# Optimization experiments

Measured on AMD Instinct MI355X. Metric: run time of the kernel, lower is better.

## Reference

```python
import jax, jax.numpy as jnp
import numpy as np

B, T, C, H, N = 2, 1024, 2048, 32, 64
LAYER_ID, N_LAYERS = 12, 24
EPS = 1e-5 * 8 ** 2  # GroupNorm eps = 1e-5 * head_size_divisor**2


def setup_inputs() -> dict:
    key = jax.random.key(0)
    ks = jax.random.split(key, 16)
    nrm = lambda i, shape, s: jax.random.normal(ks[i], shape, jnp.float32) * s
    r01 = LAYER_ID / (N_LAYERS - 1)
    r1a0 = 1.0 - LAYER_ID / N_LAYERS
    ddd = (jnp.arange(C, dtype=jnp.float32) / C)[None, None, :]
    nn_ = jnp.arange(C, dtype=jnp.float32) / (C - 1)
    decay_speed = -7.0 + 5.0 * nn_ ** (0.85 + r01 ** 0.5)
    lin_s = 1.0 / float(np.sqrt(C))
    inp = dict(
        x=nrm(0, (B, T, C), 1.0),
        v_first=nrm(1, (B, T, C), 1.0),
        shift_state=jnp.zeros((B, C), jnp.float32),
        wkv_state=jnp.zeros((B, H, N, N), jnp.float32),
        x_r=1.0 - ddd ** (0.2 * r1a0),
        x_w=1.0 - ddd ** (0.9 * r1a0),
        x_k=1.0 - (ddd ** (0.9 * r1a0) + 0.4 * r01),
        x_v=1.0 - (ddd ** (0.4 * r1a0) + 0.6 * r01),
        x_a=1.0 - ddd ** (0.9 * r1a0),
        x_g=1.0 - ddd ** (0.2 * r1a0),
        w0=decay_speed[None, None, :] + 0.5,
        w1=nrm(2, (C, 64), 0.05), w2=nrm(3, (64, C), 0.1),
        a0=jnp.zeros((1, 1, C), jnp.float32),
        a1=nrm(4, (C, 64), 0.05), a2=nrm(5, (64, C), 0.1),
        v0=jnp.ones((1, 1, C), jnp.float32),
        v1=nrm(6, (C, 32), 0.05), v2=nrm(7, (32, C), 0.1),
        g1=nrm(8, (C, 128), 0.05), g2=nrm(9, (128, C), 0.1),
        k_k=jnp.full((1, 1, C), 0.85, jnp.float32),
        k_a=jnp.ones((1, 1, C), jnp.float32),
        r_k=nrm(10, (H, N), 0.02),
        W_r=nrm(11, (C, C), lin_s), W_k=nrm(12, (C, C), lin_s),
        W_v=nrm(13, (C, C), lin_s), W_o=nrm(14, (C, C), lin_s),
        ln_w=jnp.ones((C,), jnp.float32), ln_b=jnp.zeros((C,), jnp.float32),
    )
    return inp


def _forward(x, v_first, shift_state, wkv_state, x_r, x_w, x_k, x_v, x_a, x_g,
             w0, w1, w2, a0, a1, a2, v0, v1, v2, g1, g2, k_k, k_a, r_k,
             W_r, W_k, W_v, W_o, ln_w, ln_b):
    # token shift
    xx = jnp.concatenate([shift_state[:, None, :], x[:, :-1]], axis=1) - x
    xr, xw, xk, xv, xa, xg = (x + xx * m for m in (x_r, x_w, x_k, x_v, x_a, x_g))
    r = xr @ W_r
    k = xk @ W_k
    v = xv @ W_v
    # log-decay (strictly negative)
    w_log = -jax.nn.softplus(-(w0 + jnp.tanh(xw @ w1) @ w2)) - 0.5
    # residual value mixing towards layer-0 v (layer_id > 0 branch)
    v = v + (v_first - v) * jax.nn.sigmoid(v0 + xv @ v1 @ v2)
    a = jax.nn.sigmoid(a0 + xa @ a1 @ a2)
    g = jax.nn.sigmoid(xg @ g1) @ g2
    # per-head L2-normalized removal key
    kk = (k * k_k).reshape(B, T, H, N)
    kk = kk / jnp.maximum(jnp.linalg.norm(kk, axis=-1, keepdims=True), 1e-12)
    k2 = k * (1.0 + (a - 1.0) * k_a)
    # time-major [T,B,H,N] for the scan
    tm = lambda t: t.reshape(B, T, H, N).transpose(1, 0, 2, 3)
    rs, ks_, vs = tm(r), tm(k2), tm(v)
    ws = jnp.exp(tm(w_log))               # per-channel decay in (0,1)
    a_in = -kk.transpose(1, 0, 2, 3)      # removal direction
    b_in = (kk * a.reshape(B, T, H, N)).transpose(1, 0, 2, 3)
    def step(S, t):  # S: [B,H,Nv,Nk]
        r_, k_, v_, w_, a_, b_ = t
        sa = jnp.einsum('bhvk,bhk->bhv', S, a_)
        S = S * w_[:, :, None, :] \
            + jnp.einsum('bhv,bhk->bhvk', sa, b_) \
            + jnp.einsum('bhv,bhk->bhvk', v_, k_)
        return S, jnp.einsum('bhvk,bhk->bhv', S, r_)
    S_final, o = jax.lax.scan(step, wkv_state, (rs, ks_, vs, ws, a_in, b_in))
    o = o.transpose(1, 0, 2, 3)           # [B,T,H,N]
    # GroupNorm with H groups over C channels (per-head normalization)
    mu = o.mean(-1, keepdims=True)
    var = ((o - mu) ** 2).mean(-1, keepdims=True)
    on = ((o - mu) / jnp.sqrt(var + EPS)).reshape(B, T, C) * ln_w + ln_b
    # rkv bonus term
    rr, kr, vr = r.reshape(B, T, H, N), k2.reshape(B, T, H, N), v.reshape(B, T, H, N)
    bonus = ((rr * kr * r_k).sum(-1, keepdims=True) * vr).reshape(B, T, C)
    out = ((on + bonus) * g) @ W_o
    return out


def reference(x, v_first, shift_state, wkv_state, x_r, x_w, x_k, x_v, x_a, x_g,
              w0, w1, w2, a0, a1, a2, v0, v1, v2, g1, g2, k_k, k_a, r_k,
              W_r, W_k, W_v, W_o, ln_w, ln_b):
    return _forward(x, v_first, shift_state, wkv_state, x_r, x_w, x_k, x_v, x_a, x_g,
                    w0, w1, w2, a0, a1, a2, v0, v1, v2, g1, g2, k_k, k_a, r_k,
                    W_r, W_k, W_v, W_o, ln_w, ln_b)
```

## Files before the change

### kernel.cpp

```cpp
#include <hip/hip_runtime.h>
#include <cstdint>
#include <cstddef>


#define DI __device__ __forceinline__
static constexpr int T_ = 1024, C_ = 2048, H_ = 32;

typedef __attribute__((ext_vector_type(8))) __bf16 bf16x8;
typedef __attribute__((ext_vector_type(4))) float f32x4;
typedef __attribute__((ext_vector_type(8))) unsigned short us8v;
typedef __attribute__((ext_vector_type(4))) unsigned short us4v;
typedef __attribute__((ext_vector_type(2))) unsigned short us2v;

DI float sig_(float z) { return 1.0f / (1.0f + expf(-z)); }

DI unsigned short f2bf(float f) {
  union { float f; uint32_t u; } v; v.f = f;
  uint32_t u = v.u;
  return (unsigned short)((u + 0x7FFFu + ((u >> 16) & 1u)) >> 16);
}
DI float bf2f(unsigned short h) {
  union { uint32_t u; float f; } v; v.u = ((uint32_t)h) << 16;
  return v.f;
}

DI float dpp_xor1_add(float x) {
  int r = __builtin_amdgcn_update_dpp(0, __float_as_int(x), 0xB1, 0xF, 0xF, true);
  return x + __int_as_float(r);
}
DI float dpp_xor2_add(float x) {
  int r = __builtin_amdgcn_update_dpp(0, __float_as_int(x), 0x4E, 0xF, 0xF, true);
  return x + __int_as_float(r);
}
DI float dpp_hm_add(float x) {
  int r = __builtin_amdgcn_update_dpp(0, __float_as_int(x), 0x141, 0xF, 0xF, true);
  return x + __int_as_float(r);
}

DI void gload16(const float* g, float* l) {
  __builtin_amdgcn_global_load_lds(
      (const __attribute__((address_space(1))) uint32_t*)g,
      (__attribute__((address_space(3))) uint32_t*)l, 16, 0, 0);
}
DI void gload16u(const unsigned short* g, unsigned short* l) {
  __builtin_amdgcn_global_load_lds(
      (const __attribute__((address_space(1))) uint32_t*)g,
      (__attribute__((address_space(3))) uint32_t*)l, 16, 0, 0);
}
DI void gload4(const float* g, float* l) {
  __builtin_amdgcn_global_load_lds(
      (const __attribute__((address_space(1))) uint32_t*)g,
      (__attribute__((address_space(3))) uint32_t*)l, 4, 0, 0);
}

struct Job {
  const float* A; const float* W; float* C; const float* bias;
  const float* mixv; const float* x; const float* shift;
  int N, K, ntn, aact, epi, tile_end;
};
struct Jobs { Job j[7]; };

__global__ __launch_bounds__(256) void gemm_oracle(Jobs P) {
  __shared__ float As[64][33];
  __shared__ float Ws[32][65];
  int bx = blockIdx.x, ji = 0;
  while (bx >= P.j[ji].tile_end) ++ji;
  Job J = P.j[ji];
  int tix = bx - (ji ? P.j[ji - 1].tile_end : 0);
  int mt = tix / J.ntn, nt = tix % J.ntn;
  int m0 = mt * 64, n0 = nt * 64;
  int tid = threadIdx.x, tx = tid & 15, ty = tid >> 4;
  float acc[4][4] = {};
  for (int k0 = 0; k0 < J.K; k0 += 32) {
    #pragma unroll
    for (int p = 0; p < 8; ++p) {
      int idx = p * 256 + tid;
      int r = idx >> 5, kc = idx & 31;
      int m = m0 + r, k = k0 + kc;
      float a;
      if (J.mixv) {
        float xv = J.x[(size_t)m * C_ + k];
        int t = m & (T_ - 1);
        float xp = (t == 0) ? J.shift[(size_t)(m >> 10) * C_ + k]
                            : J.x[(size_t)(m - 1) * C_ + k];
        a = xv + (xp - xv) * J.mixv[k];
      } else {
        a = J.A[(size_t)m * J.K + k];
        if (J.aact == 1) a = tanhf(a);
        else if (J.aact == 2) a = sig_(a);
      }
      As[r][kc] = a;
    }
    #pragma unroll
    for (int p = 0; p < 8; ++p) {
      int idx = p * 256 + tid;
      int kr = idx >> 6, nc = idx & 63;
      int n = n0 + nc;
      Ws[kr][nc] = (n < J.N) ? J.W[(size_t)(k0 + kr) * J.N + n] : 0.0f;
    }
    __syncthreads();
    #pragma unroll 4
    for (int kc = 0; kc < 32; ++kc) {
      float av[4], bv[4];
      #pragma unroll
      for (int i = 0; i < 4; ++i) av[i] = As[ty * 4 + i][kc];
      #pragma unroll
      for (int jn = 0; jn < 4; ++jn) bv[jn] = Ws[kc][tx * 4 + jn];
      #pragma unroll
      for (int i = 0; i < 4; ++i)
        #pragma unroll
        for (int jn = 0; jn < 4; ++jn) acc[i][jn] += av[i] * bv[jn];
    }
    __syncthreads();
  }
  #pragma unroll
  for (int i = 0; i < 4; ++i) {
    int rw = m0 + ty * 4 + i;
    #pragma unroll
    for (int jn = 0; jn < 4; ++jn) {
      int col = n0 + tx * 4 + jn;
      if (col < J.N) {
        float v = acc[i][jn];
        if (J.epi == 1) v = sig_(J.bias[col] + v);
        else if (J.epi == 2) v = 0.60653065971263342f * sig_(J.bias[col] + v);
        if (J.epi == 3) ((unsigned short*)J.C)[(size_t)rw * J.N + col] = f2bf(v);
        else            J.C[(size_t)rw * J.N + col] = v;
      }
    }
  }
}

struct TJob { const float* src; unsigned short* dh; unsigned short* dl; int N, ntn, tile_end; };
struct TJobs { TJob j[8]; };

__global__ __launch_bounds__(256) void wtrans(TJobs P) {
  __shared__ float t[64][65];
  int bx = blockIdx.x, ji = 0;
  while (bx >= P.j[ji].tile_end) ++ji;
  TJob J = P.j[ji];
  int tix = bx - (ji ? P.j[ji - 1].tile_end : 0);
  int kt = tix / J.ntn, nt = tix % J.ntn;
  int k0 = kt * 64, n0 = nt * 64;
  int tid = threadIdx.x;
  #pragma unroll
  for (int p = 0; p < 16; ++p) {
    int flat = p * 256 + tid;
    int r = flat >> 6, c = flat & 63;
    int n = n0 + c;
    t[r][c] = (n < J.N) ? J.src[(size_t)(k0 + r) * J.N + n] : 0.0f;
  }
  __syncthreads();
  #pragma unroll
  for (int p = 0; p < 8; ++p) {
    int flat = p * 256 + tid;
    int rr = flat >> 5, cc = (flat & 31) * 2;
    if (n0 + rr < J.N) {
      float w0v = t[cc][rr], w1v = t[cc + 1][rr];
      unsigned short h0 = f2bf(w0v), h1 = f2bf(w1v);
      us2v oh, ol;
      oh.x = h0; oh.y = h1;
      ol.x = f2bf(w0v - bf2f(h0));
      ol.y = f2bf(w1v - bf2f(h1));
      size_t off = (size_t)(n0 + rr) * 2048 + k0 + cc;
      *(us2v*)(J.dh + off) = oh;
      *(us2v*)(J.dl + off) = ol;
    }
  }
}

struct GJob {
  const float* A; const unsigned short* Wh; const unsigned short* Wl; float* C;
  const float* mixv; const float* shift;
  int N, K, ntn, kbeg, kend, atomicC, tile_end;
};
struct GJobs { GJob j[8]; };

__global__ __launch_bounds__(256, 2) void gemm_w256(GJobs P) {
  __shared__ unsigned short Ash[128][40];
  __shared__ unsigned short Asl[128][40];
  __shared__ unsigned short Bsh[256][32];
  __shared__ unsigned short Bsl[256][32];
  int bx = blockIdx.x, ji = 0;
  while (bx >= P.j[ji].tile_end) ++ji;
  GJob J = P.j[ji];
  int tix = bx - (ji ? P.j[ji - 1].tile_end : 0);
  int mt = tix / J.ntn, nt = tix % J.ntn;
  int m0 = mt * 128, n0 = nt * 256;
  int tid = threadIdx.x;
  int lane = tid & 63, wid = tid >> 6;
  int wr = wid >> 1, wc = wid & 1;
  int l15 = lane & 15, lg = lane >> 4;
  f32x4 acc[4][8] = {};

  int sr = tid >> 3, skq = tid & 7;
  float ax[4][4], aq[4][4], amv[4];

  auto loadA = [&](int k0) {
    int kk = k0 + skq * 4;
    if (J.mixv) *(float4*)amv = *(const float4*)(J.mixv + kk);
    #pragma unroll
    for (int p = 0; p < 4; ++p) {
      int m = m0 + p * 32 + sr;
      const float* xp0 = J.A + (size_t)m * J.K + kk;
      *(float4*)ax[p] = *(const float4*)xp0;
      if (J.mixv) {
        const float* pp = ((m & (T_ - 1)) == 0)
            ? (J.shift + (size_t)(m >> 10) * C_ + kk)
            : (xp0 - C_);
        *(float4*)aq[p] = *(const float4*)pp;
      }
    }
  };
  auto writeA = [&]() {
    #pragma unroll
    for (int p = 0; p < 4; ++p) {
      us4v oh, ol;
      #pragma unroll
      for (int q = 0; q < 4; ++q) {
        float va = J.mixv ? (ax[p][q] + (aq[p][q] - ax[p][q]) * amv[q]) : ax[p][q];
        unsigned short hq = f2bf(va);
        oh[q] = hq;
        ol[q] = f2bf(va - bf2f(hq));
      }
      int r = p * 32 + sr;
      *(us4v*)&Ash[r][skq * 4] = oh;
      *(us4v*)&Asl[r][skq * 4] = ol;
    }
  };
  auto stageB = [&](int k0) {
    #pragma unroll
    for (int j = 0; j < 4; ++j) {
      int r0 = wid * 64 + j * 16;
      int nrow = n0 + r0 + (lane >> 2);
      if (nrow >= J.N) nrow = J.N - 1;
      size_t gofs = (size_t)nrow * J.K + k0 + (lane & 3) * 8;
      gload16u(J.Wh + gofs, &Bsh[r0][0]);
      gload16u(J.Wl + gofs, &Bsl[r0][0]);
    }
  };

  loadA(J.kbeg);
  stageB(J.kbeg);
  writeA();
  asm volatile("s_waitcnt vmcnt(0)" ::: "memory");
  __syncthreads();

  for (int k0 = J.kbeg; k0 < J.kend; k0 += 32) {
    bool more = (k0 + 32 < J.kend);
    if (more) loadA(k0 + 32);
    bf16x8 afh[4], afl[4];
    #pragma unroll
    for (int i = 0; i < 4; ++i) {
      int rr = wr * 64 + i * 16 + l15;
      afh[i] = __builtin_bit_cast(bf16x8, *(const us8v*)&Ash[rr][lg * 8]);
      afl[i] = __builtin_bit_cast(bf16x8, *(const us8v*)&Asl[rr][lg * 8]);
    }
    #pragma unroll
    for (int jn = 0; jn < 8; ++jn) {
      int rb = wc * 128 + jn * 16 + l15;
      bf16x8 bh = __builtin_bit_cast(bf16x8, *(const us8v*)&Bsh[rb][lg * 8]);
      bf16x8 bl = __builtin_bit_cast(bf16x8, *(const us8v*)&Bsl[rb][lg * 8]);
      #pragma unroll
      for (int i = 0; i < 4; ++i) {
        acc[i][jn] = __builtin_amdgcn_mfma_f32_16x16x32_bf16(afh[i], bh, acc[i][jn], 0, 0, 0);
        acc[i][jn] = __builtin_amdgcn_mfma_f32_16x16x32_bf16(afl[i], bh, acc[i][jn], 0, 0, 0);
        acc[i][jn] = __builtin_amdgcn_mfma_f32_16x16x32_bf16(afh[i], bl, acc[i][jn], 0, 0, 0);
      }
    }
    __syncthreads();
    if (more) { stageB(k0 + 32); writeA(); }
    asm volatile("s_waitcnt vmcnt(0)" ::: "memory");
    __syncthreads();
  }

  int orow0 = m0 + wr * 64 + 4 * lg;
  int ocol0 = n0 + wc * 128 + l15;
  #pragma unroll
  for (int i = 0; i < 4; ++i) {
    #pragma unroll
    for (int jn = 0; jn < 8; ++jn) {
      int col = ocol0 + jn * 16;
      if (col < J.N) {
        #pragma unroll
        for (int rr = 0; rr < 4; ++rr) {
          size_t idx = (size_t)(orow0 + i * 16 + rr) * J.N + col;
          float v = acc[i][jn][rr];
          if (J.atomicC) atomicAdd(&J.C[idx], v);
          else           J.C[idx] = v;
        }
      }
    }
  }
}

__global__ __launch_bounds__(64) void prescan(
    float* __restrict__ kio, float* __restrict__ vio,
    float* __restrict__ amat_ain, float* __restrict__ vmix_bin,
    const float* __restrict__ vfirst,
    const float* __restrict__ k_k, const float* __restrict__ k_a) {
  __shared__ float red[64];
  int bid = blockIdx.x, tid = threadIdx.x;
  int h = bid & (H_ - 1);
  size_t base = (size_t)bid * 64 + tid;
  int cc = h * 64 + tid;
  float kv = kio[base];
  float kkv = kv * k_k[cc];
  red[tid] = kkv * kkv;
  __syncthreads();
  for (int s = 32; s > 0; s >>= 1) { if (tid < s) red[tid] += red[tid + s]; __syncthreads(); }
  float nrm = fmaxf(sqrtf(red[0]), 1e-12f);
  float kkn = kkv / nrm;
  float av = amat_ain[base];
  float vmv = vmix_bin[base];
  float vv = vio[base];
  kio[base] = kv * (1.0f + (av - 1.0f) * k_a[cc]);
  vio[base] = vv + (vfirst[base] - vv) * vmv;
  amat_ain[base] = -kkn;
  vmix_bin[base] = kkn * av;
}

static constexpr int CH = 16;

#define LOADSTEP(BUF, S_, Aa, Ww, Kk, Bb, Rr, Vt)                  \
  {                                                                \
    *(float4*)&Aa[0] = *(const float4*)&lds[BUF][3][S_][kb];       \
    *(float4*)&Aa[4] = *(const float4*)&lds[BUF][3][S_][kb + 4];   \
    *(float4*)&Ww[0] = *(const float4*)&lds[BUF][2][S_][kb];       \
    *(float4*)&Ww[4] = *(const float4*)&lds[BUF][2][S_][kb + 4];   \
    *(float4*)&Kk[0] = *(const float4*)&lds[BUF][1][S_][kb];       \
    *(float4*)&Kk[4] = *(const float4*)&lds[BUF][1][S_][kb + 4];   \
    *(float4*)&Bb[0] = *(const float4*)&lds[BUF][4][S_][kb];       \
    *(float4*)&Bb[4] = *(const float4*)&lds[BUF][4][S_][kb + 4];   \
    *(float4*)&Rr[0] = *(const float4*)&lds[BUF][0][S_][kb];       \
    *(float4*)&Rr[4] = *(const float4*)&lds[BUF][0][S_][kb + 4];   \
    Vt = vtl[BUF][S_][vl];                                         \
  }

#define COMPSTEP(Aa, Ww, Kk, Bb, Rr, Vt, TIDX)                              \
  {                                                                         \
    float p0 = S[0] * Aa[0], p1 = S[1] * Aa[1];                             \
    float p2 = S[2] * Aa[2], p3 = S[3] * Aa[3];                             \
    p0 = fmaf(S[4], Aa[4], p0); p1 = fmaf(S[5], Aa[5], p1);                 \
    p2 = fmaf(S[6], Aa[6], p2); p3 = fmaf(S[7], Aa[7], p3);                 \
    float sa = (p0 + p1) + (p2 + p3);                                       \
    sa = dpp_xor1_add(sa);                                                  \
    sa = dpp_xor2_add(sa);                                                  \
    sa = dpp_hm_add(sa);                                                    \
    float y0 = 0.f, y1 = 0.f, y2 = 0.f, y3 = 0.f;                           \
    _Pragma("unroll") for (int i = 0; i < 8; i += 4) {                      \
      S[i]     = fmaf(S[i],     Ww[i],     fmaf(Vt, Kk[i],     sa * Bb[i])); \
      S[i + 1] = fmaf(S[i + 1], Ww[i + 1], fmaf(Vt, Kk[i + 1], sa * Bb[i + 1])); \
      S[i + 2] = fmaf(S[i + 2], Ww[i + 2], fmaf(Vt, Kk[i + 2], sa * Bb[i + 2])); \
      S[i + 3] = fmaf(S[i + 3], Ww[i + 3], fmaf(Vt, Kk[i + 3], sa * Bb[i + 3])); \
      y0 = fmaf(S[i], Rr[i], y0);                                           \
      y1 = fmaf(S[i + 1], Rr[i + 1], y1);                                   \
      y2 = fmaf(S[i + 2], Rr[i + 2], y2);                                   \
      y3 = fmaf(S[i + 3], Rr[i + 3], y3);                                   \
    }                                                                       \
    float y = (y0 + y1) + (y2 + y3);                                        \
    y = dpp_xor1_add(y);                                                    \
    y = dpp_xor2_add(y);                                                    \
    y = dpp_hm_add(y);                                                      \
    if (kq == 0) obf[bh + (size_t)(TIDX)*2048 + v0 + vl] = f2bf(y);         \
  }

__global__ __launch_bounds__(64) void wkv_scan_v5(
    const float* __restrict__ r, const float* __restrict__ k2,
    const float* __restrict__ w, const float* __restrict__ ain,
    const float* __restrict__ bin, const float* __restrict__ vp,
    const float* __restrict__ sInit, unsigned short* __restrict__ obf) {
  __shared__ float lds[2][5][CH][64];
  __shared__ float vtl[2][CH][8];
  int D = blockIdx.x;
  int chain = (D & 7) + 8 * (D >> 6);
  int vblk = (D >> 3) & 7;
  int b = chain >> 5, h = chain & 31;
  int v0 = vblk * 8;
  int lane = threadIdx.x;
  int vl = lane >> 3, kq = lane & 7;
  int kb = kq * 8;
  size_t bh = (size_t)(b * T_) * 2048 + (size_t)h * 64;

  float S[8];
  {
    const float* sp = sInit + (((size_t)chain * 64 + v0 + vl) * 64) + kb;
    float4 s0 = *(const float4*)(sp);
    float4 s1 = *(const float4*)(sp + 4);
    S[0] = s0.x; S[1] = s0.y; S[2] = s0.z; S[3] = s0.w;
    S[4] = s1.x; S[5] = s1.y; S[6] = s1.z; S[7] = s1.w;
  }

  const float* arr[5] = {r, k2, w, ain, bin};

  auto stage = [&](int buf, int t0) {
    #pragma unroll
    for (int a = 0; a < 5; ++a) {
      #pragma unroll
      for (int jj = 0; jj < 4; ++jj) {
        size_t gofs = bh + (size_t)(t0 + jj * 4 + (lane >> 4)) * 2048 + (lane & 15) * 4;
        gload16(arr[a] + gofs, &lds[buf][a][jj * 4][0]);
      }
    }
    #pragma unroll
    for (int di = 0; di < 2; ++di) {
      size_t gofs = bh + (size_t)(t0 + di * 8 + (lane >> 3)) * 2048 + v0 + (lane & 7);
      gload4(vp + gofs, &vtl[buf][di * 8][0]);
    }
  };

  stage(0, 0);
  asm volatile("s_waitcnt vmcnt(0)" ::: "memory");

  float A0[8], W0[8], K0[8], B0[8], R0[8], vt0;
  float A1[8], W1[8], K1[8], B1[8], R1[8], vt1;

  for (int c = 0; c < T_ / CH; ++c) {
    int cur = c & 1;
    if (c + 1 < T_ / CH) stage(cur ^ 1, (c + 1) * CH);
    int t0 = c * CH;
    LOADSTEP(cur, 0, A0, W0, K0, B0, R0, vt0);
    #pragma unroll 2
    for (int s = 0; s < CH; s += 2) {
      LOADSTEP(cur, s + 1, A1, W1, K1, B1, R1, vt1);
      COMPSTEP(A0, W0, K0, B0, R0, vt0, t0 + s);
      if (s + 2 < CH) LOADSTEP(cur, s + 2, A0, W0, K0, B0, R0, vt0);
      COMPSTEP(A1, W1, K1, B1, R1, vt1, t0 + s + 1);
    }
    asm volatile("s_waitcnt vmcnt(0)" ::: "memory");
  }
}

__global__ __launch_bounds__(64) void post(
    const unsigned short* __restrict__ obf, const float* __restrict__ r,
    const float* __restrict__ k2, const float* __restrict__ vp,
    const unsigned short* __restrict__ gbf, const float* __restrict__ r_k,
    const float* __restrict__ lnw, const float* __restrict__ lnb,
    float* __restrict__ afin) {
  __shared__ float red[64];
  int bid = blockIdx.x, tid = threadIdx.x;
  int h = bid & 31;
  size_t base = (size_t)bid * 64 + tid;
  int cc = h * 64 + tid;
  float ov = bf2f(obf[base]);
  red[tid] = ov; __syncthreads();
  for (int s = 32; s > 0; s >>= 1) { if (tid < s) red[tid] += red[tid + s]; __syncthreads(); }
  float mu = red[0] * (1.0f / 64.0f);
  __syncthreads();
  float dv = ov - mu;
  red[tid] = dv * dv; __syncthreads();
  for (int s = 32; s > 0; s >>= 1) { if (tid < s) red[tid] += red[tid + s]; __syncthreads(); }
  float var = red[0] * (1.0f / 64.0f);
  __syncthreads();
  float on = dv * rsqrtf(var + 6.4e-4f) * lnw[cc] + lnb[cc];
  float pr = r[base] * k2[base] * r_k[cc];
  red[tid] = pr; __syncthreads();
  for (int s = 32; s > 0; s >>= 1) { if (tid < s) red[tid] += red[tid + s]; __syncthreads(); }
  float dot = red[0];
  float val = (on + dot * vp[base]) * bf2f(gbf[base]);
  afin[base] = val;
}

static constexpr size_t KB = 1024;
static constexpr size_t O_R    = 0;
static constexpr size_t O_K    = 16384;
static constexpr size_t O_V    = 32768;
static constexpr size_t O_WDEC = 49152;
static constexpr size_t O_AMAT = 65536;
static constexpr size_t O_VMIX = 81920;
static constexpr size_t O_AIN  = O_AMAT;
static constexpr size_t O_BIN  = O_VMIX;
static constexpr size_t O_AFIN = O_VMIX;
static constexpr size_t O_WRT_H = 49152, O_WRT_L = 57344;
static constexpr size_t O_WKT_H = 65536, O_WKT_L = 73728;
static constexpr size_t O_WVT_H = 81920, O_WVT_L = 90112;
static constexpr size_t O_W1T_H = 98304, O_W1T_L = 98560;
static constexpr size_t O_A1T_H = 98816, O_A1T_L = 99072;
static constexpr size_t O_V1T_H = 99328, O_V1T_L = 99456;
static constexpr size_t O_G1T_H = 99584, O_G1T_L = 100096;
static constexpr size_t O_WOT_H = 0, O_WOT_L = 8192;

extern "C" void kernel_launch(void* const* d_in, const int* in_sizes, int n_in,
                              void* d_out, int out_size, void* d_ws, size_t ws_size,
                              hipStream_t stream) {
  const float* x      = (const float*)d_in[0];
  const float* vfirst = (const float*)d_in[1];
  const float* shift  = (const float*)d_in[2];
  const float* wkv0   = (const float*)d_in[3];
  const float* x_r = (const float*)d_in[4];
  const float* x_w = (const float*)d_in[5];
  const float* x_k = (const float*)d_in[6];
  const float* x_v = (const float*)d_in[7];
  const float* x_a = (const float*)d_in[8];
  const float* x_g = (const float*)d_in[9];
  const float* w0 = (const float*)d_in[10];
  const float* w1 = (const float*)d_in[11];
  const float* w2 = (const float*)d_in[12];
  const float* a0 = (const float*)d_in[13];
  const float* a1 = (const float*)d_in[14];
  const float* a2 = (const float*)d_in[15];
  const float* v0 = (const float*)d_in[16];
  const float* v1 = (const float*)d_in[17];
  const float* v2 = (const float*)d_in[18];
  const float* g1 = (const float*)d_in[19];
  const float* g2 = (const float*)d_in[20];
  const float* k_k = (const float*)d_in[21];
  const float* k_a = (const float*)d_in[22];
  const float* r_k = (const float*)d_in[23];
  const float* W_r = (const float*)d_in[24];
  const float* W_k = (const float*)d_in[25];
  const float* W_v = (const float*)d_in[26];
  const float* W_o = (const float*)d_in[27];
  const float* ln_w = (const float*)d_in[28];
  const float* ln_b = (const float*)d_in[29];

  char* ws = (char*)d_ws;
  auto F = [&](size_t kb) { return (float*)(ws + kb * KB); };
  auto U = [&](size_t kb) { return (unsigned short*)(ws + kb * KB); };
  float* outp = (float*)d_out;
  unsigned short* gbf = (unsigned short*)d_out;
  unsigned short* obf = (unsigned short*)((char*)d_out + 8192 * KB);
  float* HW2 = (float*)((char*)d_out + 8192 * KB);
  float* HA2 = (float*)((char*)d_out + 8704 * KB);
  float* HV2 = (float*)((char*)d_out + 9216 * KB);
  float* HG2 = (float*)((char*)d_out + 9472 * KB);

  {
    TJobs TG{};
    int cum = 0, i = 0;
    auto addT = [&](const float* src, size_t hkb, size_t lkb, int N) {
      int ntn = (N + 63) / 64;
      cum += 32 * ntn;
      TG.j[i++] = TJob{src, U(hkb), U(lkb), N, ntn, cum};
    };
    addT(W_r, O_WRT_H, O_WRT_L, 2048);
    addT(W_k, O_WKT_H, O_WKT_L, 2048);
    addT(W_v, O_WVT_H, O_WVT_L, 2048);
    addT(w1, O_W1T_H, O_W1T_L, 64);
    addT(a1, O_A1T_H, O_A1T_L, 64);
    addT(v1, O_V1T_H, O_V1T_L, 32);
    addT(g1, O_G1T_H, O_G1T_L, 128);
    wtrans<<<dim3(cum), dim3(256), 0, stream>>>(TG);
  }

  {
    GJobs G{};
    int cum = 0, i = 0;
    auto add = [&](size_t hkb, size_t lkb, float* Cp, const float* mixv, int N) {
      int ntn = (N + 255) / 256;
      cum += 16 * ntn;
      G.j[i++] = GJob{x, U(hkb), U(lkb), Cp, mixv, shift, N, 2048, ntn, 0, 2048, 0, cum};
    };
    add(O_WRT_H, O_WRT_L, F(O_R), x_r, 2048);
    add(O_WKT_H, O_WKT_L, F(O_K), x_k, 2048);
    add(O_WVT_H, O_WVT_L, F(O_V), x_v, 2048);
    add(O_W1T_H, O_W1T_L, HW2, x_w, 64);
    add(O_A1T_H, O_A1T_L, HA2, x_a, 64);
    add(O_V1T_H, O_V1T_L, HV2, x_v, 32);
    add(O_G1T_H, O_G1T_L, HG2, x_g, 128);
    gemm_w256<<<dim3(cum), dim3(256), 0, stream>>>(G);
  }

  {
    Jobs G{};
    int cum = 0, i = 0;
    auto add = [&](const float* A, const float* W, float* C, const float* bias,
                   int K, int aact, int epi) {
      cum += 32 * 32;
      G.j[i++] = Job{A, W, C, bias, nullptr, nullptr, nullptr, 2048, K, 32, aact, epi, cum};
    };
    add(HW2, w2, F(O_WDEC), w0, 64, 1, 2);
    add(HA2, a2, F(O_AMAT), a0, 64, 0, 1);
    add(HV2, v2, F(O_VMIX), v0, 32, 0, 1);
    add(HG2, g2, (float*)gbf, nullptr, 128, 2, 3);
    gemm_oracle<<<dim3(cum), dim3(256), 0, stream>>>(G);
  }

  prescan<<<dim3(65536), dim3(64), 0, stream>>>(F(O_K), F(O_V), F(O_AMAT), F(O_VMIX),
                                                vfirst, k_k, k_a);

  wkv_scan_v5<<<dim3(512), dim3(64), 0, stream>>>(F(O_R), F(O_K), F(O_WDEC), F(O_AIN),
                                                  F(O_BIN), F(O_V), wkv0, obf);

  post<<<dim3(65536), dim3(64), 0, stream>>>(obf, F(O_R), F(O_K), F(O_V),
                                             gbf, r_k, ln_w, ln_b, F(O_AFIN));

  hipMemsetAsync(d_out, 0, (size_t)16384 * KB, stream);

  {
    TJobs TO{};
    TO.j[0] = TJob{W_o, U(O_WOT_H), U(O_WOT_L), 2048, 32, 1024};
    wtrans<<<dim3(1024), dim3(256), 0, stream>>>(TO);
  }

  {
    GJobs G{};
    G.j[0] = GJob{F(O_AFIN), U(O_WOT_H), U(O_WOT_L), outp, nullptr, nullptr,
                  2048, 2048, 8, 0, 1024, 1, 128};
    G.j[1] = GJob{F(O_AFIN), U(O_WOT_H), U(O_WOT_L), outp, nullptr, nullptr,
                  2048, 2048, 8, 1024, 2048, 1, 256};
    gemm_w256<<<dim3(256), dim3(256), 0, stream>>>(G);
  }

  (void)in_sizes; (void)n_in; (void)out_size; (void)ws_size;
}
```

Before: 866.2 us.

## Split WKV scan across more blocks with four state columns per lane

The recurrent WKV scan now gives each wave 4 value rows instead of 8, with 16 lanes each holding 4 key entries, and launches 1024 single-wave blocks instead of 512. The per-step serial chain per lane gets shorter (4 FMAs instead of 8) and more CUs run in parallel on the latency-bound scan. The cost is one extra DPP reduction stage per step, each chunk's inputs being loaded twice as many times overall, and a chunk size halved to 8, which doubles the number of barrier/waitcnt points.

```diff
diff --git a/kernel.cpp b/kernel.cpp
--- a/kernel.cpp
+++ b/kernel.cpp
@@ -34,6 +34,10 @@
 }
 DI float dpp_hm_add(float x) {
   int r = __builtin_amdgcn_update_dpp(0, __float_as_int(x), 0x141, 0xF, 0xF, true);
+  return x + __int_as_float(r);
+}
+DI float dpp_mir_add(float x) {
+  int r = __builtin_amdgcn_update_dpp(0, __float_as_int(x), 0x140, 0xF, 0xF, true);
   return x + __int_as_float(r);
 }
 
@@ -319,75 +323,65 @@
   vmix_bin[base] = kkn * av;
 }
 
-static constexpr int CH = 16;
+static constexpr int CH = 8;
 
 #define LOADSTEP(BUF, S_, Aa, Ww, Kk, Bb, Rr, Vt)                  \
   {                                                                \
     *(float4*)&Aa[0] = *(const float4*)&lds[BUF][3][S_][kb];       \
-    *(float4*)&Aa[4] = *(const float4*)&lds[BUF][3][S_][kb + 4];   \
     *(float4*)&Ww[0] = *(const float4*)&lds[BUF][2][S_][kb];       \
-    *(float4*)&Ww[4] = *(const float4*)&lds[BUF][2][S_][kb + 4];   \
     *(float4*)&Kk[0] = *(const float4*)&lds[BUF][1][S_][kb];       \
-    *(float4*)&Kk[4] = *(const float4*)&lds[BUF][1][S_][kb + 4];   \
     *(float4*)&Bb[0] = *(const float4*)&lds[BUF][4][S_][kb];       \
-    *(float4*)&Bb[4] = *(const float4*)&lds[BUF][4][S_][kb + 4];   \
     *(float4*)&Rr[0] = *(const float4*)&lds[BUF][0][S_][kb];       \
-    *(float4*)&Rr[4] = *(const float4*)&lds[BUF][0][S_][kb + 4];   \
     Vt = vtl[BUF][S_][vl];                                         \
   }
 
 #define COMPSTEP(Aa, Ww, Kk, Bb, Rr, Vt, TIDX)                              \
   {                                                                         \
     float p0 = S[0] * Aa[0], p1 = S[1] * Aa[1];                             \
-    float p2 = S[2] * Aa[2], p3 = S[3] * Aa[3];                             \
-    p0 = fmaf(S[4], Aa[4], p0); p1 = fmaf(S[5], Aa[5], p1);                 \
-    p2 = fmaf(S[6], Aa[6], p2); p3 = fmaf(S[7], Aa[7], p3);                 \
-    float sa = (p0 + p1) + (p2 + p3);                                       \
+    p0 = fmaf(S[2], Aa[2], p0);                                             \
+    p1 = fmaf(S[3], Aa[3], p1);                                             \
+    float sa = p0 + p1;                                                     \
     sa = dpp_xor1_add(sa);                                                  \
     sa = dpp_xor2_add(sa);                                                  \
     sa = dpp_hm_add(sa);                                                    \
-    float y0 = 0.f, y1 = 0.f, y2 = 0.f, y3 = 0.f;                           \
-    _Pragma("unroll") for (int i = 0; i < 8; i += 4) {                      \
-      S[i]     = fmaf(S[i],     Ww[i],     fmaf(Vt, Kk[i],     sa * Bb[i])); \
-      S[i + 1] = fmaf(S[i + 1], Ww[i + 1], fmaf(Vt, Kk[i + 1], sa * Bb[i + 1])); \
-      S[i + 2] = fmaf(S[i + 2], Ww[i + 2], fmaf(Vt, Kk[i + 2], sa * Bb[i + 2])); \
-      S[i + 3] = fmaf(S[i + 3], Ww[i + 3], fmaf(Vt, Kk[i + 3], sa * Bb[i + 3])); \
-      y0 = fmaf(S[i], Rr[i], y0);                                           \
-      y1 = fmaf(S[i + 1], Rr[i + 1], y1);                                   \
-      y2 = fmaf(S[i + 2], Rr[i + 2], y2);                                   \
-      y3 = fmaf(S[i + 3], Rr[i + 3], y3);                                   \
-    }                                                                       \
-    float y = (y0 + y1) + (y2 + y3);                                        \
+    sa = dpp_mir_add(sa);                                                   \
+    S[0] = fmaf(S[0], Ww[0], fmaf(Vt, Kk[0], sa * Bb[0]));                  \
+    S[1] = fmaf(S[1], Ww[1], fmaf(Vt, Kk[1], sa * Bb[1]));                  \
+    S[2] = fmaf(S[2], Ww[2], fmaf(Vt, Kk[2], sa * Bb[2]));                  \
+    S[3] = fmaf(S[3], Ww[3], fmaf(Vt, Kk[3], sa * Bb[3]));                  \
+    float y0 = S[0] * Rr[0], y1 = S[1] * Rr[1];                             \
+    y0 = fmaf(S[2], Rr[2], y0);                                             \
+    y1 = fmaf(S[3], Rr[3], y1);                                             \
+    float y = y0 + y1;                                                      \
     y = dpp_xor1_add(y);                                                    \
     y = dpp_xor2_add(y);                                                    \
     y = dpp_hm_add(y);                                                      \
+    y = dpp_mir_add(y);                                                     \
     if (kq == 0) obf[bh + (size_t)(TIDX)*2048 + v0 + vl] = f2bf(y);         \
   }
 
-__global__ __launch_bounds__(64) void wkv_scan_v5(
+__global__ __launch_bounds__(64) void wkv_scan_v6(
     const float* __restrict__ r, const float* __restrict__ k2,
     const float* __restrict__ w, const float* __restrict__ ain,
     const float* __restrict__ bin, const float* __restrict__ vp,
     const float* __restrict__ sInit, unsigned short* __restrict__ obf) {
   __shared__ float lds[2][5][CH][64];
-  __shared__ float vtl[2][CH][8];
+  __shared__ float vtl[2][16][4];
   int D = blockIdx.x;
-  int chain = (D & 7) + 8 * (D >> 6);
-  int vblk = (D >> 3) & 7;
+  int chain = (D & 7) + 8 * (D >> 7);
+  int vblk = (D >> 3) & 15;
   int b = chain >> 5, h = chain & 31;
-  int v0 = vblk * 8;
+  int v0 = vblk * 4;
   int lane = threadIdx.x;
-  int vl = lane >> 3, kq = lane & 7;
-  int kb = kq * 8;
+  int vl = lane >> 4, kq = lane & 15;
+  int kb = kq * 4;
   size_t bh = (size_t)(b * T_) * 2048 + (size_t)h * 64;
 
-  float S[8];
+  float S[4];
   {
     const float* sp = sInit + (((size_t)chain * 64 + v0 + vl) * 64) + kb;
-    float4 s0 = *(const float4*)(sp);
-    float4 s1 = *(const float4*)(sp + 4);
+    float4 s0 = *(const float4*)sp;
     S[0] = s0.x; S[1] = s0.y; S[2] = s0.z; S[3] = s0.w;
-    S[4] = s1.x; S[5] = s1.y; S[6] = s1.z; S[7] = s1.w;
   }
 
   const float* arr[5] = {r, k2, w, ain, bin};
@@ -396,23 +390,24 @@
     #pragma unroll
     for (int a = 0; a < 5; ++a) {
       #pragma unroll
-      for (int jj = 0; jj < 4; ++jj) {
+      for (int jj = 0; jj < 2; ++jj) {
         size_t gofs = bh + (size_t)(t0 + jj * 4 + (lane >> 4)) * 2048 + (lane & 15) * 4;
         gload16(arr[a] + gofs, &lds[buf][a][jj * 4][0]);
       }
     }
-    #pragma unroll
-    for (int di = 0; di < 2; ++di) {
-      size_t gofs = bh + (size_t)(t0 + di * 8 + (lane >> 3)) * 2048 + v0 + (lane & 7);
-      gload4(vp + gofs, &vtl[buf][di * 8][0]);
+    {
+      int tt = t0 + (lane >> 2);
+      if (tt > T_ - 1) tt = T_ - 1;
+      size_t gofs = bh + (size_t)tt * 2048 + v0 + (lane & 3);
+      gload4(vp + gofs, &vtl[buf][0][0]);
     }
   };
 
   stage(0, 0);
   asm volatile("s_waitcnt vmcnt(0)" ::: "memory");
 
-  float A0[8], W0[8], K0[8], B0[8], R0[8], vt0;
-  float A1[8], W1[8], K1[8], B1[8], R1[8], vt1;
+  float A0[4], W0[4], K0[4], B0[4], R0[4], vt0;
+  float A1[4], W1[4], K1[4], B1[4], R1[4], vt1;
 
   for (int c = 0; c < T_ / CH; ++c) {
     int cur = c & 1;
@@ -578,8 +573,8 @@
   prescan<<<dim3(65536), dim3(64), 0, stream>>>(F(O_K), F(O_V), F(O_AMAT), F(O_VMIX),
                                                 vfirst, k_k, k_a);
 
-  wkv_scan_v5<<<dim3(512), dim3(64), 0, stream>>>(F(O_R), F(O_K), F(O_WDEC), F(O_AIN),
-                                                  F(O_BIN), F(O_V), wkv0, obf);
+  wkv_scan_v6<<<dim3(1024), dim3(64), 0, stream>>>(F(O_R), F(O_K), F(O_WDEC), F(O_AIN),
+                                                   F(O_BIN), F(O_V), wkv0, obf);
 
   post<<<dim3(65536), dim3(64), 0, stream>>>(obf, F(O_R), F(O_K), F(O_V),
                                              gbf, r_k, ln_w, ln_b, F(O_AFIN));
```

New measurement: 833.4 us. 1.04x faster.
